# Kernel tuning notes

Measured on AMD Instinct MI355X. Metric: run time of the kernel, lower is better.

The kernel has to match this reference:

```python
import jax, jax.numpy as jnp
from jax import lax
import numpy as np

GAMMA = 1e-4  # RBF bandwidth (init kwarg gamma)

def setup_inputs() -> dict:
    key = jax.random.key(0)
    ks = jax.random.split(key, 6)
    B, H, W = 2048, 64, 64
    P, D = 4096, 4096  # D = 4 * (H//2) * (W//2)
    NC = 10
    x = jax.random.normal(ks[0], (B, 1, H, W), dtype=jnp.float32)
    prototypes = jax.random.normal(ks[1], (P, D), dtype=jnp.float32) * 0.5
    conv_w = jax.random.normal(ks[2], (4, 1, 2, 2), dtype=jnp.float32) * 0.5
    conv_b = jax.random.normal(ks[3], (4,), dtype=jnp.float32) * 0.1
    head_w = jax.random.normal(ks[4], (NC, P), dtype=jnp.float32) * (1.0 / np.sqrt(P))
    head_b = jax.random.normal(ks[5], (NC,), dtype=jnp.float32) * 0.1
    return {"x": x, "prototypes": prototypes, "conv_w": conv_w,
            "conv_b": conv_b, "head_w": head_w, "head_b": head_b}

def reference(x, prototypes, conv_w, conv_b, head_w, head_b):
    # 2x2 stride-2 conv: [B,1,H,W] -> [B,4,H/2,W/2]
    feats = lax.conv_general_dilated(
        x, conv_w, window_strides=(2, 2), padding="VALID",
        dimension_numbers=("NCHW", "OIHW", "NCHW"))
    feats = feats + conv_b[None, :, None, None]
    B = feats.shape[0]
    feats = feats.reshape(B, -1)  # [B, D]
    # Pairwise squared distance via ||f||^2 + ||p||^2 - 2 f.p (no [B,P,D] blowup)
    f2 = jnp.sum(feats * feats, axis=1, keepdims=True)          # [B,1]
    p2 = jnp.sum(prototypes * prototypes, axis=1)[None, :]      # [1,P]
    d2 = jnp.maximum(f2 + p2 - 2.0 * feats @ prototypes.T, 0.0)  # [B,P]
    kernel_vals = jnp.exp(-GAMMA * d2)
    logits = kernel_vals @ head_w.T + head_b
    return jax.nn.log_softmax(logits, axis=-1)
```

## Files before the change

kernel.cpp:

```cpp
#include <hip/hip_runtime.h>
#include <hip/hip_bf16.h>
#include <stdint.h>

#define GAMMA 1e-4f

typedef int i32x4 __attribute__((ext_vector_type(4)));
typedef int i32x8 __attribute__((ext_vector_type(8)));
typedef float f32x4 __attribute__((ext_vector_type(4)));

__device__ __forceinline__ float bf2f(unsigned short u) {
  unsigned int x = ((unsigned int)u) << 16;
  float f; __builtin_memcpy(&f, &x, 4);
  return f;
}

__device__ __forceinline__ unsigned char f2e4m3(float x) {
  float a = fabsf(x);
  unsigned char s = x < 0.f ? 0x80 : 0;
  a = fminf(a, 448.f);
  if (a < 0.015625f) {
    int q = (int)rintf(a * 512.f);
    return s | (unsigned char)q;
  }
  unsigned int u; __builtin_memcpy(&u, &a, 4);
  u += 0x7FFFFu + ((u >> 20) & 1);
  u &= 0xFFF00000u;
  int e2 = (int)(u >> 23) - 127;
  unsigned int mant = (u >> 20) & 7;
  return s | (unsigned char)(((e2 + 7) << 3) | mant);
}

__device__ __forceinline__ unsigned int pack4(float a, float b, float c, float d) {
  return (unsigned)f2e4m3(a) | ((unsigned)f2e4m3(b) << 8) |
         ((unsigned)f2e4m3(c) << 16) | ((unsigned)f2e4m3(d) << 24);
}

__global__ __launch_bounds__(256) void prep_k(
    const float* __restrict__ x, const float* __restrict__ cw,
    const float* __restrict__ cb, unsigned char* __restrict__ fA8,
    float* __restrict__ f2, const float* __restrict__ pr,
    unsigned char* __restrict__ pB8, float* __restrict__ p2) {
  const int tid = threadIdx.x;
  __shared__ float red[4];
  if (blockIdx.x < 4096) {
    const int j = blockIdx.x;
    const float4* src = (const float4*)(pr + (size_t)j * 4096);
    float ssq = 0.f;
    unsigned int w4[4];
#pragma unroll
    for (int k = 0; k < 4; k++) {
      float4 v = src[tid * 4 + k];
      ssq += v.x * v.x + v.y * v.y + v.z * v.z + v.w * v.w;
      w4[k] = pack4(v.x, v.y, v.z, v.w);
    }
    *(uint4*)(pB8 + (size_t)j * 4096 + tid * 16) = make_uint4(w4[0], w4[1], w4[2], w4[3]);
    for (int off = 32; off > 0; off >>= 1) ssq += __shfl_down(ssq, off);
    if ((tid & 63) == 0) red[tid >> 6] = ssq;
    __syncthreads();
    if (tid == 0) p2[j] = red[0] + red[1] + red[2] + red[3];
  } else {
    const int b = blockIdx.x - 4096;
    __shared__ float swb[20];
    if (tid < 16) swb[tid] = cw[tid];
    else if (tid < 20) swb[tid] = cb[tid - 16];
    __syncthreads();
    float w[16], bias[4];
#pragma unroll
    for (int i = 0; i < 16; i++) w[i] = swb[i];
#pragma unroll
    for (int c = 0; c < 4; c++) bias[c] = swb[16 + c];
    const float* xb = x + (size_t)b * 4096;
    unsigned char* fb8 = fA8 + (size_t)b * 4096;
    const int p0 = tid * 4;
    const int h = p0 >> 5, w0 = p0 & 31;
    const float* r0 = xb + (2 * h) * 64 + 2 * w0;
    const float* r1 = r0 + 64;
    float4 a0 = *(const float4*)r0, a1 = *(const float4*)(r0 + 4);
    float4 c0 = *(const float4*)r1, c1 = *(const float4*)(r1 + 4);
    float ssq = 0.f;
#pragma unroll
    for (int c = 0; c < 4; c++) {
      float w00 = w[c * 4], w01 = w[c * 4 + 1], w10 = w[c * 4 + 2], w11 = w[c * 4 + 3];
      float v0 = bias[c] + a0.x * w00 + a0.y * w01 + c0.x * w10 + c0.y * w11;
      float v1 = bias[c] + a0.z * w00 + a0.w * w01 + c0.z * w10 + c0.w * w11;
      float v2 = bias[c] + a1.x * w00 + a1.y * w01 + c1.x * w10 + c1.y * w11;
      float v3 = bias[c] + a1.z * w00 + a1.w * w01 + c1.z * w10 + c1.w * w11;
      ssq += v0 * v0 + v1 * v1 + v2 * v2 + v3 * v3;
      *(unsigned int*)(fb8 + c * 1024 + p0) = pack4(v0, v1, v2, v3);
    }
    for (int off = 32; off > 0; off >>= 1) ssq += __shfl_down(ssq, off);
    if ((tid & 63) == 0) red[tid >> 6] = ssq;
    __syncthreads();
    if (tid == 0) f2[b] = red[0] + red[1] + red[2] + red[3];
  }
}

#define SWZ(o) ((o) ^ ((((o) >> 12) & 1) << 4))
#define TILE_BYTES 32768

#define GLDS(gsrc, ldst)                                                    \
  __builtin_amdgcn_global_load_lds(                                         \
      (__attribute__((address_space(1))) void*)(void*)(gsrc),               \
      (__attribute__((address_space(3))) void*)(ldst), 16, 0, 0)

#define MFMA8(a, b, c)                                                      \
  __builtin_amdgcn_mfma_scale_f32_16x16x128_f8f6f4(                         \
      (a), (b), (c), 0, 0, 0, 0x7f7f7f7fu, 0, 0x7f7f7f7fu)

__device__ __forceinline__ i32x8 read32(const char* p0, const char* p1) {
  i32x4 lo = *(const i32x4*)p0;
  i32x4 hi = *(const i32x4*)p1;
  return __builtin_shufflevector(lo, hi, 0, 1, 2, 3, 4, 5, 6, 7);
}

#define TBODY(CUR, NXT, KB)                                                 \
  {                                                                         \
    i32x8 av0, av1, av2, av3, bv0, bv1, bv2, bv3;                           \
    __builtin_amdgcn_sched_barrier(0);                                      \
    av0 = read32((CUR) + arlo[0], (CUR) + arhi[0]);                         \
    av1 = read32((CUR) + arlo[1], (CUR) + arhi[1]);                         \
    av2 = read32((CUR) + arlo[2], (CUR) + arhi[2]);                         \
    av3 = read32((CUR) + arlo[3], (CUR) + arhi[3]);                         \
    bv0 = read32((CUR) + brlo[0], (CUR) + brhi[0]);                         \
    bv1 = read32((CUR) + brlo[1], (CUR) + brhi[1]);                         \
    __builtin_amdgcn_sched_barrier(0);                                      \
    GLDS(agp[0] + (KB), (NXT) + aoff[0]);                                   \
    GLDS(agp[1] + (KB), (NXT) + aoff[1]);                                   \
    GLDS(agp[2] + (KB), (NXT) + aoff[2]);                                   \
    GLDS(agp[3] + (KB), (NXT) + aoff[3]);                                   \
    bv2 = read32((CUR) + brlo[2], (CUR) + brhi[2]);                         \
    bv3 = read32((CUR) + brlo[3], (CUR) + brhi[3]);                         \
    GLDS(bgp[0] + (KB), (NXT) + 16384 + boff[0]);                           \
    GLDS(bgp[1] + (KB), (NXT) + 16384 + boff[1]);                           \
    GLDS(bgp[2] + (KB), (NXT) + 16384 + boff[2]);                           \
    GLDS(bgp[3] + (KB), (NXT) + 16384 + boff[3]);                           \
    __builtin_amdgcn_sched_barrier(0);                                      \
    asm volatile("s_waitcnt lgkmcnt(4)" ::: "memory");                      \
    __builtin_amdgcn_sched_barrier(0);                                      \
    __builtin_amdgcn_s_setprio(1);                                          \
    acc[0][0] = MFMA8(av0, bv0, acc[0][0]);                                 \
    acc[0][1] = MFMA8(av0, bv1, acc[0][1]);                                 \
    acc[1][0] = MFMA8(av1, bv0, acc[1][0]);                                 \
    acc[1][1] = MFMA8(av1, bv1, acc[1][1]);                                 \
    acc[2][0] = MFMA8(av2, bv0, acc[2][0]);                                 \
    acc[2][1] = MFMA8(av2, bv1, acc[2][1]);                                 \
    acc[3][0] = MFMA8(av3, bv0, acc[3][0]);                                 \
    acc[3][1] = MFMA8(av3, bv1, acc[3][1]);                                 \
    __builtin_amdgcn_s_setprio(0);                                          \
    __builtin_amdgcn_sched_barrier(0);                                      \
    asm volatile("s_waitcnt lgkmcnt(0)" ::: "memory");                      \
    __builtin_amdgcn_sched_barrier(0);                                      \
    __builtin_amdgcn_s_setprio(1);                                          \
    acc[0][2] = MFMA8(av0, bv2, acc[0][2]);                                 \
    acc[0][3] = MFMA8(av0, bv3, acc[0][3]);                                 \
    acc[1][2] = MFMA8(av1, bv2, acc[1][2]);                                 \
    acc[1][3] = MFMA8(av1, bv3, acc[1][3]);                                 \
    acc[2][2] = MFMA8(av2, bv2, acc[2][2]);                                 \
    acc[2][3] = MFMA8(av2, bv3, acc[2][3]);                                 \
    acc[3][2] = MFMA8(av3, bv2, acc[3][2]);                                 \
    acc[3][3] = MFMA8(av3, bv3, acc[3][3]);                                 \
    __builtin_amdgcn_s_setprio(0);                                          \
    __builtin_amdgcn_sched_barrier(0);                                      \
    asm volatile("s_waitcnt vmcnt(0)" ::: "memory");                        \
    __builtin_amdgcn_sched_barrier(0);                                      \
    __builtin_amdgcn_s_barrier();                                           \
  }

__global__ __launch_bounds__(256, 2) void gemm_kv_k(
    const unsigned char* __restrict__ A, const unsigned char* __restrict__ B,
    const float* __restrict__ f2, const float* __restrict__ p2,
    __hip_bfloat16* __restrict__ kv) {
  __shared__ __align__(16) char lds[2 * TILE_BYTES];
  const int tid = threadIdx.x;
  const int wave = tid >> 6, lane = tid & 63;
  const int q = lane >> 4, l16 = lane & 15;
  const int wr = wave >> 1, wc = wave & 1;

  const int wg = blockIdx.x;
  const int xcd = wg & 7, loc = wg >> 3;
  const int bm = loc >> 2;
  const int bn = xcd * 4 + (loc & 3);

  const unsigned char* agp[4];
  const unsigned char* bgp[4];
  int aoff[4], boff[4];
#pragma unroll
  for (int i = 0; i < 4; i++) {
    int phys = (tid + i * 256) * 16;
    aoff[i] = phys;
    boff[i] = phys;
    int lg = SWZ(phys);
    int kq = lg >> 12, rw = (lg & 4095) >> 5, kl = lg & 31;
    agp[i] = A + (size_t)(bm * 128 + rw) * 4096 + kq * 32 + kl;
    bgp[i] = B + (size_t)(bn * 128 + rw) * 4096 + kq * 32 + kl;
  }

  int arlo[4], arhi[4], brlo[4], brhi[4];
#pragma unroll
  for (int m = 0; m < 4; m++) {
    int lg = q * 4096 + (wr * 64 + m * 16 + l16) * 32;
    arlo[m] = SWZ(lg);
    arhi[m] = SWZ(lg + 16);
  }
#pragma unroll
  for (int n = 0; n < 4; n++) {
    int lg = q * 4096 + (wc * 64 + n * 16 + l16) * 32;
    brlo[n] = 16384 + SWZ(lg);
    brhi[n] = 16384 + SWZ(lg + 16);
  }

  f32x4 acc[4][4] = {};

  char* buf0 = lds;
  char* buf1 = lds + TILE_BYTES;

#pragma unroll
  for (int i = 0; i < 4; i++) GLDS(agp[i], buf0 + aoff[i]);
#pragma unroll
  for (int i = 0; i < 4; i++) GLDS(bgp[i], buf0 + 16384 + boff[i]);
  asm volatile("s_waitcnt vmcnt(0)" ::: "memory");
  __builtin_amdgcn_s_barrier();

#pragma unroll 1
  for (int t = 0; t < 32; t += 2) {
    const int kb1 = ((t + 1) & 31) * 128;
    const int kb2 = ((t + 2) & 31) * 128;
    TBODY(buf0, buf1, kb1);
    TBODY(buf1, buf0, kb2);
  }

  float p2v[4];
#pragma unroll
  for (int n = 0; n < 4; n++) p2v[n] = p2[bn * 128 + wc * 64 + n * 16 + l16];
#pragma unroll
  for (int m = 0; m < 4; m++) {
#pragma unroll
    for (int j = 0; j < 4; j++) {
      int grow = bm * 128 + wr * 64 + m * 16 + q * 4 + j;
      float f2v = f2[grow];
      __hip_bfloat16* kvp = kv + (size_t)grow * 4096 + bn * 128 + wc * 64 + l16;
#pragma unroll
      for (int n = 0; n < 4; n++) {
        float d2 = fmaxf(f2v + p2v[n] - 2.0f * acc[m][n][j], 0.f);
        kvp[n * 16] = __float2bfloat16(__expf(-GAMMA * d2));
      }
    }
  }
}

__global__ __launch_bounds__(256) void head_ls_k(
    const __hip_bfloat16* __restrict__ kv, const float* __restrict__ hw,
    const float* __restrict__ hb, float* __restrict__ out) {
  const int bb = blockIdx.x * 8;
  const int tid = threadIdx.x;
  float part[8][10];
#pragma unroll
  for (int r = 0; r < 8; r++)
#pragma unroll
    for (int c = 0; c < 10; c++) part[r][c] = 0.f;
#pragma unroll
  for (int k = 0; k < 4; k++) {
    int idx = tid + k * 256;
    float4 w[10];
#pragma unroll
    for (int c = 0; c < 10; c++) w[c] = *(const float4*)(hw + c * 4096 + idx * 4);
#pragma unroll
    for (int r = 0; r < 8; r++) {
      ushort4 v = ((const ushort4*)(kv + (size_t)(bb + r) * 4096))[idx];
      float a0 = bf2f(v.x), a1 = bf2f(v.y), a2 = bf2f(v.z), a3 = bf2f(v.w);
#pragma unroll
      for (int c = 0; c < 10; c++)
        part[r][c] += a0 * w[c].x + a1 * w[c].y + a2 * w[c].z + a3 * w[c].w;
    }
  }
#pragma unroll
  for (int r = 0; r < 8; r++)
#pragma unroll
    for (int c = 0; c < 10; c++)
      for (int off = 32; off > 0; off >>= 1) part[r][c] += __shfl_down(part[r][c], off);
  __shared__ float red[4][8][10];
  if ((tid & 63) == 0) {
#pragma unroll
    for (int r = 0; r < 8; r++)
#pragma unroll
      for (int c = 0; c < 10; c++) red[tid >> 6][r][c] = part[r][c];
  }
  __syncthreads();
  if (tid < 8) {
    const int r = tid;
    float l[10], m = -1e30f;
#pragma unroll
    for (int c = 0; c < 10; c++) {
      l[c] = red[0][r][c] + red[1][r][c] + red[2][r][c] + red[3][r][c] + hb[c];
      m = fmaxf(m, l[c]);
    }
    float s = 0.f;
#pragma unroll
    for (int c = 0; c < 10; c++) s += __expf(l[c] - m);
    float lse = logf(s);
#pragma unroll
    for (int c = 0; c < 10; c++) out[(size_t)(bb + r) * 10 + c] = l[c] - m - lse;
  }
}

extern "C" void kernel_launch(void* const* d_in, const int* in_sizes, int n_in,
                              void* d_out, int out_size, void* d_ws, size_t ws_size,
                              hipStream_t stream) {
  const float* x      = (const float*)d_in[0];
  const float* protos = (const float*)d_in[1];
  const float* conv_w = (const float*)d_in[2];
  const float* conv_b = (const float*)d_in[3];
  const float* head_w = (const float*)d_in[4];
  const float* head_b = (const float*)d_in[5];
  float* out = (float*)d_out;
  char* ws = (char*)d_ws;

  unsigned char* pB8  = (unsigned char*)ws;
  unsigned char* fA8  = (unsigned char*)(ws + (16u << 20));
  __hip_bfloat16* kvb = (__hip_bfloat16*)(ws + (24u << 20));
  float* f2 = (float*)(ws + (40u << 20));
  float* p2 = (float*)(ws + (40u << 20) + 8192);

  hipLaunchKernelGGL(prep_k, dim3(6144), dim3(256), 0, stream,
                     x, conv_w, conv_b, fA8, f2, protos, pB8, p2);
  hipLaunchKernelGGL(gemm_kv_k, dim3(512), dim3(256), 0, stream, fA8, pB8, f2, p2, kvb);
  hipLaunchKernelGGL(head_ls_k, dim3(256), dim3(256), 0, stream, kvb, head_w, head_b, out);
}
```

Baseline: 92.04 us.

## Replace double-buffered GEMM pipeline with single-buffer loop and split head kernel finer

New measurement: 120.5 us. 30.9% more time.

```diff
diff --git a/kernel.cpp b/kernel.cpp
--- a/kernel.cpp
+++ b/kernel.cpp
@@ -96,7 +96,6 @@
 }
 
 #define SWZ(o) ((o) ^ ((((o) >> 12) & 1) << 4))
-#define TILE_BYTES 32768
 
 #define GLDS(gsrc, ldst)                                                    \
   __builtin_amdgcn_global_load_lds(                                         \
@@ -113,64 +112,11 @@
   return __builtin_shufflevector(lo, hi, 0, 1, 2, 3, 4, 5, 6, 7);
 }
 
-#define TBODY(CUR, NXT, KB)                                                 \
-  {                                                                         \
-    i32x8 av0, av1, av2, av3, bv0, bv1, bv2, bv3;                           \
-    __builtin_amdgcn_sched_barrier(0);                                      \
-    av0 = read32((CUR) + arlo[0], (CUR) + arhi[0]);                         \
-    av1 = read32((CUR) + arlo[1], (CUR) + arhi[1]);                         \
-    av2 = read32((CUR) + arlo[2], (CUR) + arhi[2]);                         \
-    av3 = read32((CUR) + arlo[3], (CUR) + arhi[3]);                         \
-    bv0 = read32((CUR) + brlo[0], (CUR) + brhi[0]);                         \
-    bv1 = read32((CUR) + brlo[1], (CUR) + brhi[1]);                         \
-    __builtin_amdgcn_sched_barrier(0);                                      \
-    GLDS(agp[0] + (KB), (NXT) + aoff[0]);                                   \
-    GLDS(agp[1] + (KB), (NXT) + aoff[1]);                                   \
-    GLDS(agp[2] + (KB), (NXT) + aoff[2]);                                   \
-    GLDS(agp[3] + (KB), (NXT) + aoff[3]);                                   \
-    bv2 = read32((CUR) + brlo[2], (CUR) + brhi[2]);                         \
-    bv3 = read32((CUR) + brlo[3], (CUR) + brhi[3]);                         \
-    GLDS(bgp[0] + (KB), (NXT) + 16384 + boff[0]);                           \
-    GLDS(bgp[1] + (KB), (NXT) + 16384 + boff[1]);                           \
-    GLDS(bgp[2] + (KB), (NXT) + 16384 + boff[2]);                           \
-    GLDS(bgp[3] + (KB), (NXT) + 16384 + boff[3]);                           \
-    __builtin_amdgcn_sched_barrier(0);                                      \
-    asm volatile("s_waitcnt lgkmcnt(4)" ::: "memory");                      \
-    __builtin_amdgcn_sched_barrier(0);                                      \
-    __builtin_amdgcn_s_setprio(1);                                          \
-    acc[0][0] = MFMA8(av0, bv0, acc[0][0]);                                 \
-    acc[0][1] = MFMA8(av0, bv1, acc[0][1]);                                 \
-    acc[1][0] = MFMA8(av1, bv0, acc[1][0]);                                 \
-    acc[1][1] = MFMA8(av1, bv1, acc[1][1]);                                 \
-    acc[2][0] = MFMA8(av2, bv0, acc[2][0]);                                 \
-    acc[2][1] = MFMA8(av2, bv1, acc[2][1]);                                 \
-    acc[3][0] = MFMA8(av3, bv0, acc[3][0]);                                 \
-    acc[3][1] = MFMA8(av3, bv1, acc[3][1]);                                 \
-    __builtin_amdgcn_s_setprio(0);                                          \
-    __builtin_amdgcn_sched_barrier(0);                                      \
-    asm volatile("s_waitcnt lgkmcnt(0)" ::: "memory");                      \
-    __builtin_amdgcn_sched_barrier(0);                                      \
-    __builtin_amdgcn_s_setprio(1);                                          \
-    acc[0][2] = MFMA8(av0, bv2, acc[0][2]);                                 \
-    acc[0][3] = MFMA8(av0, bv3, acc[0][3]);                                 \
-    acc[1][2] = MFMA8(av1, bv2, acc[1][2]);                                 \
-    acc[1][3] = MFMA8(av1, bv3, acc[1][3]);                                 \
-    acc[2][2] = MFMA8(av2, bv2, acc[2][2]);                                 \
-    acc[2][3] = MFMA8(av2, bv3, acc[2][3]);                                 \
-    acc[3][2] = MFMA8(av3, bv2, acc[3][2]);                                 \
-    acc[3][3] = MFMA8(av3, bv3, acc[3][3]);                                 \
-    __builtin_amdgcn_s_setprio(0);                                          \
-    __builtin_amdgcn_sched_barrier(0);                                      \
-    asm volatile("s_waitcnt vmcnt(0)" ::: "memory");                        \
-    __builtin_amdgcn_sched_barrier(0);                                      \
-    __builtin_amdgcn_s_barrier();                                           \
-  }
-
-__global__ __launch_bounds__(256, 2) void gemm_kv_k(
+__global__ __launch_bounds__(256, 4) void gemm_kv_k(
     const unsigned char* __restrict__ A, const unsigned char* __restrict__ B,
     const float* __restrict__ f2, const float* __restrict__ p2,
     __hip_bfloat16* __restrict__ kv) {
-  __shared__ __align__(16) char lds[2 * TILE_BYTES];
+  __shared__ __align__(16) char lds[32768];
   const int tid = threadIdx.x;
   const int wave = tid >> 6, lane = tid & 63;
   const int q = lane >> 4, l16 = lane & 15;
@@ -183,12 +129,11 @@
 
   const unsigned char* agp[4];
   const unsigned char* bgp[4];
-  int aoff[4], boff[4];
+  int aoff[4];
 #pragma unroll
   for (int i = 0; i < 4; i++) {
     int phys = (tid + i * 256) * 16;
     aoff[i] = phys;
-    boff[i] = phys;
     int lg = SWZ(phys);
     int kq = lg >> 12, rw = (lg & 4095) >> 5, kl = lg & 31;
     agp[i] = A + (size_t)(bm * 128 + rw) * 4096 + kq * 32 + kl;
@@ -211,22 +156,42 @@
 
   f32x4 acc[4][4] = {};
 
-  char* buf0 = lds;
-  char* buf1 = lds + TILE_BYTES;
-
-#pragma unroll
-  for (int i = 0; i < 4; i++) GLDS(agp[i], buf0 + aoff[i]);
-#pragma unroll
-  for (int i = 0; i < 4; i++) GLDS(bgp[i], buf0 + 16384 + boff[i]);
-  asm volatile("s_waitcnt vmcnt(0)" ::: "memory");
-  __builtin_amdgcn_s_barrier();
-
 #pragma unroll 1
-  for (int t = 0; t < 32; t += 2) {
-    const int kb1 = ((t + 1) & 31) * 128;
-    const int kb2 = ((t + 2) & 31) * 128;
-    TBODY(buf0, buf1, kb1);
-    TBODY(buf1, buf0, kb2);
+  for (int t = 0; t < 32; ++t) {
+    const int kb = t * 128;
+#pragma unroll
+    for (int i = 0; i < 4; i++) GLDS(agp[i] + kb, lds + aoff[i]);
+#pragma unroll
+    for (int i = 0; i < 4; i++) GLDS(bgp[i] + kb, lds + 16384 + aoff[i]);
+    __syncthreads();
+
+    i32x8 av0 = read32(lds + arlo[0], lds + arhi[0]);
+    i32x8 av1 = read32(lds + arlo[1], lds + arhi[1]);
+    i32x8 av2 = read32(lds + arlo[2], lds + arhi[2]);
+    i32x8 av3 = read32(lds + arlo[3], lds + arhi[3]);
+    i32x8 bv0 = read32(lds + brlo[0], lds + brhi[0]);
+    i32x8 bv1 = read32(lds + brlo[1], lds + brhi[1]);
+    i32x8 bv2 = read32(lds + brlo[2], lds + brhi[2]);
+    i32x8 bv3 = read32(lds + brlo[3], lds + brhi[3]);
+
+    acc[0][0] = MFMA8(av0, bv0, acc[0][0]);
+    acc[0][1] = MFMA8(av0, bv1, acc[0][1]);
+    acc[1][0] = MFMA8(av1, bv0, acc[1][0]);
+    acc[1][1] = MFMA8(av1, bv1, acc[1][1]);
+    acc[2][0] = MFMA8(av2, bv0, acc[2][0]);
+    acc[2][1] = MFMA8(av2, bv1, acc[2][1]);
+    acc[3][0] = MFMA8(av3, bv0, acc[3][0]);
+    acc[3][1] = MFMA8(av3, bv1, acc[3][1]);
+    acc[0][2] = MFMA8(av0, bv2, acc[0][2]);
+    acc[0][3] = MFMA8(av0, bv3, acc[0][3]);
+    acc[1][2] = MFMA8(av1, bv2, acc[1][2]);
+    acc[1][3] = MFMA8(av1, bv3, acc[1][3]);
+    acc[2][2] = MFMA8(av2, bv2, acc[2][2]);
+    acc[2][3] = MFMA8(av2, bv3, acc[2][3]);
+    acc[3][2] = MFMA8(av3, bv2, acc[3][2]);
+    acc[3][3] = MFMA8(av3, bv3, acc[3][3]);
+
+    __syncthreads();
   }
 
   float p2v[4];
@@ -248,45 +213,50 @@
   }
 }
 
-__global__ __launch_bounds__(256) void head_ls_k(
+__global__ __launch_bounds__(256, 4) void head_ls_k(
     const __hip_bfloat16* __restrict__ kv, const float* __restrict__ hw,
     const float* __restrict__ hb, float* __restrict__ out) {
-  const int bb = blockIdx.x * 8;
+  const int bb = blockIdx.x * 4;
   const int tid = threadIdx.x;
-  float part[8][10];
-#pragma unroll
-  for (int r = 0; r < 8; r++)
+  float part[4][10];
+#pragma unroll
+  for (int r = 0; r < 4; r++)
 #pragma unroll
     for (int c = 0; c < 10; c++) part[r][c] = 0.f;
-#pragma unroll
+
+#pragma unroll 1
   for (int k = 0; k < 4; k++) {
-    int idx = tid + k * 256;
-    float4 w[10];
-#pragma unroll
-    for (int c = 0; c < 10; c++) w[c] = *(const float4*)(hw + c * 4096 + idx * 4);
-#pragma unroll
-    for (int r = 0; r < 8; r++) {
+    const int idx = tid + k * 256;
+    float a[4][4];
+#pragma unroll
+    for (int r = 0; r < 4; r++) {
       ushort4 v = ((const ushort4*)(kv + (size_t)(bb + r) * 4096))[idx];
-      float a0 = bf2f(v.x), a1 = bf2f(v.y), a2 = bf2f(v.z), a3 = bf2f(v.w);
-#pragma unroll
-      for (int c = 0; c < 10; c++)
-        part[r][c] += a0 * w[c].x + a1 * w[c].y + a2 * w[c].z + a3 * w[c].w;
-    }
-  }
-#pragma unroll
-  for (int r = 0; r < 8; r++)
+      a[r][0] = bf2f(v.x); a[r][1] = bf2f(v.y); a[r][2] = bf2f(v.z); a[r][3] = bf2f(v.w);
+    }
+#pragma unroll
+    for (int c = 0; c < 10; c++) {
+      float4 w = *(const float4*)(hw + c * 4096 + idx * 4);
+#pragma unroll
+      for (int r = 0; r < 4; r++)
+        part[r][c] += a[r][0] * w.x + a[r][1] * w.y + a[r][2] * w.z + a[r][3] * w.w;
+    }
+  }
+
+#pragma unroll
+  for (int r = 0; r < 4; r++)
 #pragma unroll
     for (int c = 0; c < 10; c++)
       for (int off = 32; off > 0; off >>= 1) part[r][c] += __shfl_down(part[r][c], off);
-  __shared__ float red[4][8][10];
+
+  __shared__ float red[4][4][10];
   if ((tid & 63) == 0) {
 #pragma unroll
-    for (int r = 0; r < 8; r++)
+    for (int r = 0; r < 4; r++)
 #pragma unroll
       for (int c = 0; c < 10; c++) red[tid >> 6][r][c] = part[r][c];
   }
   __syncthreads();
-  if (tid < 8) {
+  if (tid < 4) {
     const int r = tid;
     float l[10], m = -1e30f;
 #pragma unroll
@@ -324,5 +294,5 @@
   hipLaunchKernelGGL(prep_k, dim3(6144), dim3(256), 0, stream,
                      x, conv_w, conv_b, fA8, f2, protos, pB8, p2);
   hipLaunchKernelGGL(gemm_kv_k, dim3(512), dim3(256), 0, stream, fA8, pB8, f2, p2, kvb);
-  hipLaunchKernelGGL(head_ls_k, dim3(256), dim3(256), 0, stream, kvb, head_w, head_b, out);
-}
+  hipLaunchKernelGGL(head_ls_k, dim3(512), dim3(256), 0, stream, kvb, head_w, head_b, out);
+}
```
